# Performance work log

Hardware: AMD Instinct MI355X
Metric: run time of the kernel (lower is better)

The kernel has to match this reference:

```python
import jax, jax.numpy as jnp
import numpy as np

B, P = 4096, 32
NUM_ENTITY = 100000
NUM_METAPATH = 3
EMBED = 128
MAX_LEN = 3
C1, C2 = 128, 32


def setup_inputs() -> dict:
    key = jax.random.key(0)
    ks = jax.random.split(key, 20)
    inp = {}
    for g, L in enumerate([1, 2, 3]):
        inp[f"ent{L}"] = jax.random.randint(ks[3 * g], (B, P, L + 1), 0, NUM_ENTITY, dtype=jnp.int32)
        inp[f"mid{L}"] = jax.random.randint(ks[3 * g + 1], (B, P, L), 0, NUM_METAPATH, dtype=jnp.int32)
        inp[f"counts{L}"] = jax.random.uniform(ks[3 * g + 2], (B, P), jnp.float32, 0.5, 1.5)
    # parameters
    inp["E"] = jax.random.normal(ks[9], (NUM_ENTITY, EMBED), jnp.float32) * 0.02
    inp["W"] = jax.random.normal(ks[10], (NUM_METAPATH, EMBED), jnp.float32) * 0.1 + 1.0
    inp["Bm"] = jax.random.normal(ks[11], (NUM_METAPATH, EMBED), jnp.float32) * 0.02
    d_in = 2 * EMBED * MAX_LEN  # 768
    inp["W1"] = jax.random.normal(ks[12], (d_in, C1), jnp.float32) * (1.0 / np.sqrt(d_in))
    inp["b1"] = jnp.zeros((C1,), jnp.float32)
    inp["W2"] = jax.random.normal(ks[13], (C1, C2), jnp.float32) * (1.0 / np.sqrt(C1))
    inp["b2"] = jnp.zeros((C2,), jnp.float32)
    inp["W3"] = jax.random.normal(ks[14], (C2, 1), jnp.float32) * (1.0 / np.sqrt(C2))
    inp["b3"] = jnp.zeros((1,), jnp.float32)
    return inp


def _group_output(E, W, Bm, ents, mids, counts):
    """Vectorized forward_path over [B, P] paths of fixed length L, then
    count-weighted average over the P paths. ents: [B,P,L+1], mids: [B,P,L]."""
    L = mids.shape[-1]
    # forward direction
    x = E[ents[..., 0]]  # [B,P,EMBED]
    y = x
    for i in range(L):
        y = E[ents[..., i + 1]]
        x = jax.nn.relu(x * W[mids[..., i]] * y + Bm[mids[..., i]])
    out1 = x
    # backward direction: original code reuses stale y (embed of last entity)
    x = E[ents[..., L]]
    for i in reversed(range(L)):
        x = jax.nn.relu(x * W[mids[..., i]] * y + Bm[mids[..., i]])
    out2 = x
    path_out = jnp.concatenate([out1, out2], axis=-1)  # [B,P,2*EMBED]
    num = jnp.einsum("bp,bpe->be", counts, path_out)
    return num / jnp.sum(counts, axis=1, keepdims=True)  # [B,2*EMBED]


def reference(ent1, mid1, ent2, mid2, ent3, mid3, counts1, counts2, counts3,
              E, W, Bm, W1, b1, W2, b2, W3, b3):
    g1 = _group_output(E, W, Bm, ent1, mid1, counts1)
    g2 = _group_output(E, W, Bm, ent2, mid2, counts2)
    g3 = _group_output(E, W, Bm, ent3, mid3, counts3)
    h = jnp.concatenate([g1, g2, g3], axis=1)  # [B, 768]
    h = jax.nn.relu(h @ W1 + b1)
    h = jax.nn.relu(h @ W2 + b2)
    return h @ W3 + b3  # [B, 1]
```

## Files before the change

### kernel.cpp

```cpp
#include <hip/hip_runtime.h>

#define EMBED 128
#define NPATH 32
#define BATCH 4096
#define DIN 768
#define C1 128
#define C2 32

__device__ __forceinline__ float sel3(float a0, float a1, float a2, int m) {
    float r = a0;
    r = (m == 1) ? a1 : r;
    r = (m == 2) ? a2 : r;
    return r;
}

__device__ __forceinline__ float4 sel3q(const float4 a[3], int m) {
    float4 r;
    r.x = sel3(a[0].x, a[1].x, a[2].x, m);
    r.y = sel3(a[0].y, a[1].y, a[2].y, m);
    r.z = sel3(a[0].z, a[1].z, a[2].z, m);
    r.w = sel3(a[0].w, a[1].w, a[2].w, m);
    return r;
}

__device__ __forceinline__ float4 chain_step(float4 x, float4 y, float4 wm, float4 bm) {
    float4 r;
    r.x = fmaxf(fmaf(x.x * wm.x, y.x, bm.x), 0.f);
    r.y = fmaxf(fmaf(x.y * wm.y, y.y, bm.y), 0.f);
    r.z = fmaxf(fmaf(x.z * wm.z, y.z, bm.z), 0.f);
    r.w = fmaxf(fmaf(x.w * wm.w, y.w, bm.w), 0.f);
    return r;
}

template<int L>
__device__ __forceinline__ void group_body(
    const int* __restrict__ ent, const int* __restrict__ mid,
    const float* __restrict__ counts, const float4* __restrict__ E4,
    const float4* __restrict__ W4, const float4* __restrict__ B4,
    float* __restrict__ h, int gcol, int* s_idx, float4* s_red)
{
    const int b = blockIdx.x;
    const int tid = threadIdx.x;
    const int dl = tid & 31;
    const int pq = tid >> 5;

    int* s_ent = s_idx;
    int* s_mid = s_idx + NPATH * (L + 1);
    float* s_cnt = (float*)(s_idx + NPATH * (2 * L + 1));

    const int* entb = ent + (size_t)b * (NPATH * (L + 1));
    const int* midb = mid + (size_t)b * (NPATH * L);
    for (int i = tid; i < NPATH * (L + 1); i += 256) s_ent[i] = entb[i];
    for (int i = tid; i < NPATH * L; i += 256) s_mid[i] = midb[i];
    if (tid < NPATH) s_cnt[tid] = counts[(size_t)b * NPATH + tid];
    __syncthreads();

    float4 Wr[3], Br[3];
#pragma unroll
    for (int m = 0; m < 3; ++m) {
        Wr[m] = W4[m * 32 + dl];
        Br[m] = B4[m * 32 + dl];
    }

    float4 n1 = make_float4(0.f, 0.f, 0.f, 0.f);
    float4 n2 = make_float4(0.f, 0.f, 0.f, 0.f);

#pragma unroll 2
    for (int j = 0; j < NPATH / 8; ++j) {
        const int p = pq + 8 * j;
        int ei[L + 1], mi[L];
#pragma unroll
        for (int i = 0; i <= L; ++i) ei[i] = s_ent[p * (L + 1) + i];
#pragma unroll
        for (int i = 0; i < L; ++i) mi[i] = s_mid[p * L + i];

        float4 e[L + 1];
#pragma unroll
        for (int i = 0; i <= L; ++i) e[i] = E4[(size_t)ei[i] * 32 + dl];
        const float c = s_cnt[p];

        float4 x = e[0];
#pragma unroll
        for (int i = 0; i < L; ++i)
            x = chain_step(x, e[i + 1], sel3q(Wr, mi[i]), sel3q(Br, mi[i]));

        const float4 yl = e[L];
        float4 x2 = yl;
#pragma unroll
        for (int i = L - 1; i >= 0; --i)
            x2 = chain_step(x2, yl, sel3q(Wr, mi[i]), sel3q(Br, mi[i]));

        n1.x = fmaf(c, x.x, n1.x); n1.y = fmaf(c, x.y, n1.y);
        n1.z = fmaf(c, x.z, n1.z); n1.w = fmaf(c, x.w, n1.w);
        n2.x = fmaf(c, x2.x, n2.x); n2.y = fmaf(c, x2.y, n2.y);
        n2.z = fmaf(c, x2.z, n2.z); n2.w = fmaf(c, x2.w, n2.w);
    }

    s_red[(pq * 2 + 0) * 32 + dl] = n1;
    s_red[(pq * 2 + 1) * 32 + dl] = n2;
    __syncthreads();
    if (tid < 64) {
        const int half = tid >> 5, dq = tid & 31;
        float4 a = s_red[(0 * 2 + half) * 32 + dq];
#pragma unroll
        for (int q = 1; q < 8; ++q) {
            float4 t = s_red[(q * 2 + half) * 32 + dq];
            a.x += t.x; a.y += t.y; a.z += t.z; a.w += t.w;
        }
        float den = 0.f;
#pragma unroll
        for (int p = 0; p < NPATH; ++p) den += s_cnt[p];
        const float inv = 1.f / den;
        a.x *= inv; a.y *= inv; a.z *= inv; a.w *= inv;
        float4* hb = (float4*)(h + (size_t)b * DIN + gcol);
        hb[half * 32 + dq] = a;
    }
}

__global__ __launch_bounds__(256) void groups_kernel(
    const int* __restrict__ e1, const int* __restrict__ m1, const float* __restrict__ c1,
    const int* __restrict__ e2, const int* __restrict__ m2, const float* __restrict__ c2,
    const int* __restrict__ e3, const int* __restrict__ m3, const float* __restrict__ c3,
    const float* __restrict__ E, const float* __restrict__ W, const float* __restrict__ Bm,
    float* __restrict__ h)
{
    __shared__ int s_idx[NPATH * 7 + NPATH];
    __shared__ float4 s_red[8 * 2 * 32];
    const float4* E4 = (const float4*)E;
    const float4* W4 = (const float4*)W;
    const float4* B4 = (const float4*)Bm;
    const int g = blockIdx.y;
    if (g == 0)      group_body<1>(e1, m1, c1, E4, W4, B4, h, 0,   s_idx, s_red);
    else if (g == 1) group_body<2>(e2, m2, c2, E4, W4, B4, h, 256, s_idx, s_red);
    else             group_body<3>(e3, m3, c3, E4, W4, B4, h, 512, s_idx, s_red);
}

#define MROWS 8
__global__ __launch_bounds__(256) void mlp_kernel(
    const float* __restrict__ h,
    const float* __restrict__ W1, const float* __restrict__ b1,
    const float* __restrict__ W2, const float* __restrict__ b2,
    const float* __restrict__ W3, const float* __restrict__ b3,
    float* __restrict__ out)
{
    const int tid = threadIdx.x;
    const int c = tid & 127;
    const int rh = tid >> 7;
    const int row0 = blockIdx.x * MROWS;

    __shared__ float hs[MROWS * DIN];
    {
        const float4* src = (const float4*)(h + (size_t)row0 * DIN);
        float4* dst = (float4*)hs;
#pragma unroll
        for (int i = 0; i < (MROWS * DIN / 4) / 256; ++i)
            dst[tid + i * 256] = src[tid + i * 256];
    }
    __syncthreads();

    float acc[4];
    const float bias1 = b1[c];
#pragma unroll
    for (int r = 0; r < 4; ++r) acc[r] = bias1;

    const float* hrow = hs + rh * 4 * DIN;
    for (int k0 = 0; k0 < DIN; k0 += 4) {
        float w0 = W1[(k0 + 0) * C1 + c];
        float w1 = W1[(k0 + 1) * C1 + c];
        float w2 = W1[(k0 + 2) * C1 + c];
        float w3 = W1[(k0 + 3) * C1 + c];
#pragma unroll
        for (int r = 0; r < 4; ++r) {
            const float4 hq = *(const float4*)(hrow + r * DIN + k0);
            acc[r] = fmaf(hq.x, w0, acc[r]);
            acc[r] = fmaf(hq.y, w1, acc[r]);
            acc[r] = fmaf(hq.z, w2, acc[r]);
            acc[r] = fmaf(hq.w, w3, acc[r]);
        }
    }

    __shared__ float h1[MROWS][C1];
#pragma unroll
    for (int r = 0; r < 4; ++r) h1[rh * 4 + r][c] = fmaxf(acc[r], 0.f);
    __syncthreads();

    __shared__ float h2[MROWS][C2];
    {
        const int r = tid >> 5;
        const int c2 = tid & 31;
        float a = b2[c2];
#pragma unroll
        for (int k = 0; k < C1; ++k)
            a = fmaf(h1[r][k], W2[k * C2 + c2], a);
        h2[r][c2] = fmaxf(a, 0.f);
    }
    __syncthreads();

    if (tid < MROWS) {
        float a = b3[0];
#pragma unroll
        for (int k = 0; k < C2; ++k)
            a = fmaf(h2[tid][k], W3[k], a);
        out[row0 + tid] = a;
    }
}

extern "C" void kernel_launch(void* const* d_in, const int* in_sizes, int n_in,
                              void* d_out, int out_size, void* d_ws, size_t ws_size,
                              hipStream_t stream) {
    const int*   ent1 = (const int*)d_in[0];
    const int*   mid1 = (const int*)d_in[1];
    const float* cnt1 = (const float*)d_in[2];
    const int*   ent2 = (const int*)d_in[3];
    const int*   mid2 = (const int*)d_in[4];
    const float* cnt2 = (const float*)d_in[5];
    const int*   ent3 = (const int*)d_in[6];
    const int*   mid3 = (const int*)d_in[7];
    const float* cnt3 = (const float*)d_in[8];
    const float* E    = (const float*)d_in[9];
    const float* W    = (const float*)d_in[10];
    const float* Bm   = (const float*)d_in[11];
    const float* W1   = (const float*)d_in[12];
    const float* b1   = (const float*)d_in[13];
    const float* W2   = (const float*)d_in[14];
    const float* b2   = (const float*)d_in[15];
    const float* W3   = (const float*)d_in[16];
    const float* b3   = (const float*)d_in[17];

    float* h = (float*)d_ws;
    float* out = (float*)d_out;

    dim3 ggrid(BATCH, 3);
    groups_kernel<<<ggrid, 256, 0, stream>>>(ent1, mid1, cnt1, ent2, mid2, cnt2,
                                             ent3, mid3, cnt3, E, W, Bm, h);
    mlp_kernel<<<BATCH / MROWS, 256, 0, stream>>>(h, W1, b1, W2, b2, W3, b3, out);
}
```

Measured before the change: 215.6 us.

## Fuse path-group aggregation and MLP into one kernel per row pair

Merges the groups kernel and the MLP kernel into a single kernel where each block processes two batch rows, running all three path groups sequentially and then the MLP on the shared-memory features. This drops the global round-trip of the 768-wide hidden vector and one kernel launch. In exchange the grid shrinks from 12288 blocks to 2048, each block serialises six group passes with extra barriers, and W1 is re-read per two rows instead of per eight, which raises L2 traffic for the first layer.

```diff
diff --git a/kernel.cpp b/kernel.cpp
--- a/kernel.cpp
+++ b/kernel.cpp
@@ -6,6 +6,7 @@
 #define DIN 768
 #define C1 128
 #define C2 32
+#define RROWS 2
 
 __device__ __forceinline__ float sel3(float a0, float a1, float a2, int m) {
     float r = a0;
@@ -34,12 +35,11 @@
 
 template<int L>
 __device__ __forceinline__ void group_body(
-    const int* __restrict__ ent, const int* __restrict__ mid,
+    int b, const int* __restrict__ ent, const int* __restrict__ mid,
     const float* __restrict__ counts, const float4* __restrict__ E4,
-    const float4* __restrict__ W4, const float4* __restrict__ B4,
-    float* __restrict__ h, int gcol, int* s_idx, float4* s_red)
+    const float4 Wr[3], const float4 Br[3],
+    float* hdst, int gcol, int* s_idx, float4* s_red)
 {
-    const int b = blockIdx.x;
     const int tid = threadIdx.x;
     const int dl = tid & 31;
     const int pq = tid >> 5;
@@ -55,13 +55,6 @@
     if (tid < NPATH) s_cnt[tid] = counts[(size_t)b * NPATH + tid];
     __syncthreads();
 
-    float4 Wr[3], Br[3];
-#pragma unroll
-    for (int m = 0; m < 3; ++m) {
-        Wr[m] = W4[m * 32 + dl];
-        Br[m] = B4[m * 32 + dl];
-    }
-
     float4 n1 = make_float4(0.f, 0.f, 0.f, 0.f);
     float4 n2 = make_float4(0.f, 0.f, 0.f, 0.f);
 
@@ -112,96 +105,88 @@
         for (int p = 0; p < NPATH; ++p) den += s_cnt[p];
         const float inv = 1.f / den;
         a.x *= inv; a.y *= inv; a.z *= inv; a.w *= inv;
-        float4* hb = (float4*)(h + (size_t)b * DIN + gcol);
+        float4* hb = (float4*)(hdst + gcol);
         hb[half * 32 + dq] = a;
     }
-}
-
-__global__ __launch_bounds__(256) void groups_kernel(
+    __syncthreads();
+}
+
+__global__ __launch_bounds__(256) void fused_kernel(
     const int* __restrict__ e1, const int* __restrict__ m1, const float* __restrict__ c1,
     const int* __restrict__ e2, const int* __restrict__ m2, const float* __restrict__ c2,
     const int* __restrict__ e3, const int* __restrict__ m3, const float* __restrict__ c3,
     const float* __restrict__ E, const float* __restrict__ W, const float* __restrict__ Bm,
-    float* __restrict__ h)
-{
-    __shared__ int s_idx[NPATH * 7 + NPATH];
-    __shared__ float4 s_red[8 * 2 * 32];
-    const float4* E4 = (const float4*)E;
-    const float4* W4 = (const float4*)W;
-    const float4* B4 = (const float4*)Bm;
-    const int g = blockIdx.y;
-    if (g == 0)      group_body<1>(e1, m1, c1, E4, W4, B4, h, 0,   s_idx, s_red);
-    else if (g == 1) group_body<2>(e2, m2, c2, E4, W4, B4, h, 256, s_idx, s_red);
-    else             group_body<3>(e3, m3, c3, E4, W4, B4, h, 512, s_idx, s_red);
-}
-
-#define MROWS 8
-__global__ __launch_bounds__(256) void mlp_kernel(
-    const float* __restrict__ h,
     const float* __restrict__ W1, const float* __restrict__ b1,
     const float* __restrict__ W2, const float* __restrict__ b2,
     const float* __restrict__ W3, const float* __restrict__ b3,
     float* __restrict__ out)
 {
+    __shared__ int s_idx[NPATH * 7 + NPATH];
+    __shared__ float4 s_red[8 * 2 * 32];
+    __shared__ float hs[RROWS * DIN];
+    __shared__ float h1s[RROWS][C1];
+    __shared__ float h2s[RROWS][C2];
+
+    const float4* E4 = (const float4*)E;
+    const float4* W4 = (const float4*)W;
+    const float4* B4 = (const float4*)Bm;
     const int tid = threadIdx.x;
-    const int c = tid & 127;
-    const int rh = tid >> 7;
-    const int row0 = blockIdx.x * MROWS;
-
-    __shared__ float hs[MROWS * DIN];
+    const int dl = tid & 31;
+
+    float4 Wr[3], Br[3];
+#pragma unroll
+    for (int m = 0; m < 3; ++m) {
+        Wr[m] = W4[m * 32 + dl];
+        Br[m] = B4[m * 32 + dl];
+    }
+
+    const int b0 = blockIdx.x * RROWS;
+    for (int r = 0; r < RROWS; ++r) {
+        const int b = b0 + r;
+        float* hrow = hs + r * DIN;
+        group_body<1>(b, e1, m1, c1, E4, Wr, Br, hrow, 0,   s_idx, s_red);
+        group_body<2>(b, e2, m2, c2, E4, Wr, Br, hrow, 256, s_idx, s_red);
+        group_body<3>(b, e3, m3, c3, E4, Wr, Br, hrow, 512, s_idx, s_red);
+    }
+
     {
-        const float4* src = (const float4*)(h + (size_t)row0 * DIN);
-        float4* dst = (float4*)hs;
-#pragma unroll
-        for (int i = 0; i < (MROWS * DIN / 4) / 256; ++i)
-            dst[tid + i * 256] = src[tid + i * 256];
-    }
-    __syncthreads();
-
-    float acc[4];
-    const float bias1 = b1[c];
-#pragma unroll
-    for (int r = 0; r < 4; ++r) acc[r] = bias1;
-
-    const float* hrow = hs + rh * 4 * DIN;
-    for (int k0 = 0; k0 < DIN; k0 += 4) {
-        float w0 = W1[(k0 + 0) * C1 + c];
-        float w1 = W1[(k0 + 1) * C1 + c];
-        float w2 = W1[(k0 + 2) * C1 + c];
-        float w3 = W1[(k0 + 3) * C1 + c];
-#pragma unroll
-        for (int r = 0; r < 4; ++r) {
-            const float4 hq = *(const float4*)(hrow + r * DIN + k0);
-            acc[r] = fmaf(hq.x, w0, acc[r]);
-            acc[r] = fmaf(hq.y, w1, acc[r]);
-            acc[r] = fmaf(hq.z, w2, acc[r]);
-            acc[r] = fmaf(hq.w, w3, acc[r]);
+        const int c = tid & 127;
+        const int rh = tid >> 7;
+        float acc = b1[c];
+        const float* hrow = hs + rh * DIN;
+#pragma unroll 4
+        for (int k0 = 0; k0 < DIN; k0 += 4) {
+            float w0 = W1[(k0 + 0) * C1 + c];
+            float w1 = W1[(k0 + 1) * C1 + c];
+            float w2 = W1[(k0 + 2) * C1 + c];
+            float w3 = W1[(k0 + 3) * C1 + c];
+            const float4 hq = *(const float4*)(hrow + k0);
+            acc = fmaf(hq.x, w0, acc);
+            acc = fmaf(hq.y, w1, acc);
+            acc = fmaf(hq.z, w2, acc);
+            acc = fmaf(hq.w, w3, acc);
         }
-    }
-
-    __shared__ float h1[MROWS][C1];
-#pragma unroll
-    for (int r = 0; r < 4; ++r) h1[rh * 4 + r][c] = fmaxf(acc[r], 0.f);
-    __syncthreads();
-
-    __shared__ float h2[MROWS][C2];
-    {
-        const int r = tid >> 5;
-        const int c2 = tid & 31;
-        float a = b2[c2];
+        h1s[rh][c] = fmaxf(acc, 0.f);
+    }
+    __syncthreads();
+
+    if (tid < RROWS * C2) {
+        const int rr = tid >> 5;
+        const int cc = tid & 31;
+        float a = b2[cc];
 #pragma unroll
         for (int k = 0; k < C1; ++k)
-            a = fmaf(h1[r][k], W2[k * C2 + c2], a);
-        h2[r][c2] = fmaxf(a, 0.f);
-    }
-    __syncthreads();
-
-    if (tid < MROWS) {
+            a = fmaf(h1s[rr][k], W2[k * C2 + cc], a);
+        h2s[rr][cc] = fmaxf(a, 0.f);
+    }
+    __syncthreads();
+
+    if (tid < RROWS) {
         float a = b3[0];
 #pragma unroll
         for (int k = 0; k < C2; ++k)
-            a = fmaf(h2[tid][k], W3[k], a);
-        out[row0 + tid] = a;
+            a = fmaf(h2s[tid][k], W3[k], a);
+        out[b0 + tid] = a;
     }
 }
 
@@ -226,12 +211,9 @@
     const float* b2   = (const float*)d_in[15];
     const float* W3   = (const float*)d_in[16];
     const float* b3   = (const float*)d_in[17];
-
-    float* h = (float*)d_ws;
     float* out = (float*)d_out;
 
-    dim3 ggrid(BATCH, 3);
-    groups_kernel<<<ggrid, 256, 0, stream>>>(ent1, mid1, cnt1, ent2, mid2, cnt2,
-                                             ent3, mid3, cnt3, E, W, Bm, h);
-    mlp_kernel<<<BATCH / MROWS, 256, 0, stream>>>(h, W1, b1, W2, b2, W3, b3, out);
-}
+    fused_kernel<<<BATCH / RROWS, 256, 0, stream>>>(
+        ent1, mid1, cnt1, ent2, mid2, cnt2, ent3, mid3, cnt3,
+        E, W, Bm, W1, b1, W2, b2, W3, b3, out);
+}
```

Measured after the change: 229.2 us. 6.4% more time.

## Retile MLP to 64-row blocks with wave-uniform weight loads; interleave group blocks

Applied to the files above, without the earlier changes.

The MLP kernel now handles 64 rows per 512-thread block. Each thread owns one row, and each wave covers 16 output columns, so W1 and W2 reads are wave-uniform (scalar-like) loads. h is staged transposed in LDS in 256-wide K chunks. This is meant to cut the repeated W1 global traffic that came from 8-row blocks. The groups kernel grid is flattened to interleave the three path lengths, balancing work across CUs. In exchange, the MLP launches far fewer blocks (64), which may underfill the GPU and serialises a long per-thread FMA chain.

```diff
diff --git a/kernel.cpp b/kernel.cpp
--- a/kernel.cpp
+++ b/kernel.cpp
@@ -34,12 +34,11 @@
 
 template<int L>
 __device__ __forceinline__ void group_body(
-    const int* __restrict__ ent, const int* __restrict__ mid,
+    int b, const int* __restrict__ ent, const int* __restrict__ mid,
     const float* __restrict__ counts, const float4* __restrict__ E4,
     const float4* __restrict__ W4, const float4* __restrict__ B4,
     float* __restrict__ h, int gcol, int* s_idx, float4* s_red)
 {
-    const int b = blockIdx.x;
     const int tid = threadIdx.x;
     const int dl = tid & 31;
     const int pq = tid >> 5;
@@ -129,78 +128,94 @@
     const float4* E4 = (const float4*)E;
     const float4* W4 = (const float4*)W;
     const float4* B4 = (const float4*)Bm;
-    const int g = blockIdx.y;
-    if (g == 0)      group_body<1>(e1, m1, c1, E4, W4, B4, h, 0,   s_idx, s_red);
-    else if (g == 1) group_body<2>(e2, m2, c2, E4, W4, B4, h, 256, s_idx, s_red);
-    else             group_body<3>(e3, m3, c3, E4, W4, B4, h, 512, s_idx, s_red);
-}
-
-#define MROWS 8
-__global__ __launch_bounds__(256) void mlp_kernel(
+    const int bx = blockIdx.x;
+    const int g = bx % 3;
+    const int b = bx / 3;
+    if (g == 0)      group_body<1>(b, e1, m1, c1, E4, W4, B4, h, 0,   s_idx, s_red);
+    else if (g == 1) group_body<2>(b, e2, m2, c2, E4, W4, B4, h, 256, s_idx, s_red);
+    else             group_body<3>(b, e3, m3, c3, E4, W4, B4, h, 512, s_idx, s_red);
+}
+
+#define MB 64
+#define KC 256
+__global__ __launch_bounds__(512) void mlp_kernel(
     const float* __restrict__ h,
     const float* __restrict__ W1, const float* __restrict__ b1,
     const float* __restrict__ W2, const float* __restrict__ b2,
     const float* __restrict__ W3, const float* __restrict__ b3,
     float* __restrict__ out)
 {
+    __shared__ float hs[KC * MB];
+    __shared__ float h1s[C1 * MB];
+    __shared__ float h2s[C2 * MB];
+
     const int tid = threadIdx.x;
-    const int c = tid & 127;
-    const int rh = tid >> 7;
-    const int row0 = blockIdx.x * MROWS;
-
-    __shared__ float hs[MROWS * DIN];
+    const int r = tid & 63;
+    const int w = __builtin_amdgcn_readfirstlane(tid >> 6);
+    const int row0 = blockIdx.x * MB;
+
+    const int cbase = w * 16;
+    float acc[16];
+#pragma unroll
+    for (int j = 0; j < 16; ++j) acc[j] = b1[cbase + j];
+
+    for (int ch = 0; ch < DIN / KC; ++ch) {
+        const int k0 = ch * KC;
+        {
+            const int tr = tid >> 3;
+            const int tc = tid & 7;
+#pragma unroll
+            for (int i = 0; i < KC / 32; ++i) {
+                const int kl = i * 32 + tc * 4;
+                const float4 v = *(const float4*)(h + (size_t)(row0 + tr) * DIN + k0 + kl);
+                hs[(kl + 0) * MB + tr] = v.x;
+                hs[(kl + 1) * MB + tr] = v.y;
+                hs[(kl + 2) * MB + tr] = v.z;
+                hs[(kl + 3) * MB + tr] = v.w;
+            }
+        }
+        __syncthreads();
+
+        const float* w1p = W1 + (size_t)k0 * C1 + cbase;
+#pragma unroll 4
+        for (int k = 0; k < KC; ++k) {
+            const float hk = hs[k * MB + r];
+            const float* w1k = w1p + (size_t)k * C1;
+#pragma unroll
+            for (int j = 0; j < 16; ++j)
+                acc[j] = fmaf(hk, w1k[j], acc[j]);
+        }
+        __syncthreads();
+    }
+
+#pragma unroll
+    for (int j = 0; j < 16; ++j)
+        h1s[(cbase + j) * MB + r] = fmaxf(acc[j], 0.f);
+    __syncthreads();
+
     {
-        const float4* src = (const float4*)(h + (size_t)row0 * DIN);
-        float4* dst = (float4*)hs;
-#pragma unroll
-        for (int i = 0; i < (MROWS * DIN / 4) / 256; ++i)
-            dst[tid + i * 256] = src[tid + i * 256];
-    }
-    __syncthreads();
-
-    float acc[4];
-    const float bias1 = b1[c];
-#pragma unroll
-    for (int r = 0; r < 4; ++r) acc[r] = bias1;
-
-    const float* hrow = hs + rh * 4 * DIN;
-    for (int k0 = 0; k0 < DIN; k0 += 4) {
-        float w0 = W1[(k0 + 0) * C1 + c];
-        float w1 = W1[(k0 + 1) * C1 + c];
-        float w2 = W1[(k0 + 2) * C1 + c];
-        float w3 = W1[(k0 + 3) * C1 + c];
-#pragma unroll
-        for (int r = 0; r < 4; ++r) {
-            const float4 hq = *(const float4*)(hrow + r * DIN + k0);
-            acc[r] = fmaf(hq.x, w0, acc[r]);
-            acc[r] = fmaf(hq.y, w1, acc[r]);
-            acc[r] = fmaf(hq.z, w2, acc[r]);
-            acc[r] = fmaf(hq.w, w3, acc[r]);
-        }
-    }
-
-    __shared__ float h1[MROWS][C1];
-#pragma unroll
-    for (int r = 0; r < 4; ++r) h1[rh * 4 + r][c] = fmaxf(acc[r], 0.f);
-    __syncthreads();
-
-    __shared__ float h2[MROWS][C2];
-    {
-        const int r = tid >> 5;
-        const int c2 = tid & 31;
-        float a = b2[c2];
-#pragma unroll
-        for (int k = 0; k < C1; ++k)
-            a = fmaf(h1[r][k], W2[k * C2 + c2], a);
-        h2[r][c2] = fmaxf(a, 0.f);
-    }
-    __syncthreads();
-
-    if (tid < MROWS) {
+        const int c2b = w * 4;
+        float a2[4];
+#pragma unroll
+        for (int j = 0; j < 4; ++j) a2[j] = b2[c2b + j];
+        for (int k = 0; k < C1; ++k) {
+            const float hk = h1s[k * MB + r];
+            const float* w2k = W2 + (size_t)k * C2 + c2b;
+#pragma unroll
+            for (int j = 0; j < 4; ++j)
+                a2[j] = fmaf(hk, w2k[j], a2[j]);
+        }
+#pragma unroll
+        for (int j = 0; j < 4; ++j)
+            h2s[(c2b + j) * MB + r] = fmaxf(a2[j], 0.f);
+    }
+    __syncthreads();
+
+    if (tid < MB) {
         float a = b3[0];
 #pragma unroll
         for (int k = 0; k < C2; ++k)
-            a = fmaf(h2[tid][k], W3[k], a);
+            a = fmaf(h2s[k * MB + tid], W3[k], a);
         out[row0 + tid] = a;
     }
 }
@@ -230,8 +245,7 @@
     float* h = (float*)d_ws;
     float* out = (float*)d_out;
 
-    dim3 ggrid(BATCH, 3);
-    groups_kernel<<<ggrid, 256, 0, stream>>>(ent1, mid1, cnt1, ent2, mid2, cnt2,
-                                             ent3, mid3, cnt3, E, W, Bm, h);
-    mlp_kernel<<<BATCH / MROWS, 256, 0, stream>>>(h, W1, b1, W2, b2, W3, b3, out);
-}
+    groups_kernel<<<3 * BATCH, 256, 0, stream>>>(ent1, mid1, cnt1, ent2, mid2, cnt2,
+                                                 ent3, mid3, cnt3, E, W, Bm, h);
+    mlp_kernel<<<BATCH / MB, 512, 0, stream>>>(h, W1, b1, W2, b2, W3, b3, out);
+}
```

Result: slower. 263.1 us (+22.1%).
